# Kernel tuning notes

Measured on AMD Instinct MI355X. Metric: run time of the kernel, lower is better.

The kernel has to match this reference:

```python
import jax, jax.numpy as jnp
import numpy as np

N_NODES = 100000
N_EDGES = 1600000
IN_DIM = 128
EM_DIM = 64
HI_DIM = 64
OUT_DIM = 128
HEADS = 4


def setup_inputs() -> dict:
    key = jax.random.key(0)
    ks = jax.random.split(key, 16)
    s = 0.05  # small init scale to keep exp(a) well-conditioned
    return {
        "x_from": jax.random.normal(ks[0], (N_NODES, IN_DIM), jnp.float32),
        "edge_index": jax.random.randint(ks[1], (2, N_EDGES), 0, N_NODES, jnp.int32),
        "Wi1": jax.random.normal(ks[2], (HEADS, IN_DIM, EM_DIM), jnp.float32) * s,
        "bi1": jax.random.normal(ks[3], (HEADS, EM_DIM), jnp.float32) * s,
        "Wi2": jax.random.normal(ks[4], (HEADS, EM_DIM, EM_DIM), jnp.float32) * s,
        "bi2": jax.random.normal(ks[5], (HEADS, EM_DIM), jnp.float32) * s,
        "Wa1": jax.random.normal(ks[6], (HEADS, 2 * EM_DIM, HI_DIM), jnp.float32) * s,
        "ba1": jax.random.normal(ks[7], (HEADS, HI_DIM), jnp.float32) * s,
        "Wa2": jax.random.normal(ks[8], (HEADS, HI_DIM, 1), jnp.float32) * s,
        "ba2": jax.random.normal(ks[9], (HEADS, 1), jnp.float32) * s,
        "Wf1": jax.random.normal(ks[10], (HEADS * EM_DIM, HI_DIM), jnp.float32) * s,
        "bf1": jax.random.normal(ks[11], (HI_DIM,), jnp.float32) * s,
        "Wf2": jax.random.normal(ks[12], (HI_DIM, OUT_DIM), jnp.float32) * s,
        "bf2": jax.random.normal(ks[13], (OUT_DIM,), jnp.float32) * s,
    }


def reference(x_from, edge_index, Wi1, bi1, Wi2, bi2, Wa1, ba1, Wa2, ba2,
              Wf1, bf1, Wf2, bf2):
    n = x_from.shape[0]
    src, dst = edge_index[0], edge_index[1]

    # per-head node embedding MLP (layer_n=2, leaky_relu between layers)
    h1 = jax.nn.leaky_relu(jnp.einsum('nf,hfe->hne', x_from, Wi1) + bi1[:, None, :])
    hs = jnp.einsum('hne,hed->hnd', h1, Wi2) + bi2[:, None, :]  # [H, N, EM]
    # hs_to in the original is f_init(x_from) again -> identical to hs

    em = hs.shape[-1]
    # A(cat(h_src, h_dst)) first linear split per-node to avoid [H,E,2*EM] cat
    s_src = jnp.einsum('hne,hek->hnk', hs, Wa1[:, :em, :])  # [H, N, HI]
    s_dst = jnp.einsum('hne,hek->hnk', hs, Wa1[:, em:, :])  # [H, N, HI]
    t = jax.nn.leaky_relu(s_src[:, src] + s_dst[:, dst] + ba1[:, None, :])  # [H, E, HI]
    a = jax.nn.leaky_relu(jnp.einsum('hek,hko->heo', t, Wa2) + ba2[:, None, :])  # [H,E,1]

    e = jnp.exp(a)  # [H, E, 1]
    # softmax denominator is scatter_add over SRC (as in the source)
    e_sum = jax.vmap(lambda v: jax.ops.segment_sum(v, src, num_segments=n))(e)  # [H,N,1]
    alpha = e / e_sum[:, src]  # [H, E, 1]

    # attention-weighted aggregation: scatter_add of hs[src]*alpha onto dst
    msg = hs[:, src] * alpha  # [H, E, EM]
    agg = jax.vmap(lambda v: jax.ops.segment_sum(v, dst, num_segments=n))(msg)  # [H,N,EM]

    h_cat = jnp.transpose(agg, (1, 0, 2)).reshape(n, -1)  # [N, H*EM], head-major cat
    out = jax.nn.leaky_relu(h_cat @ Wf1 + bf1) @ Wf2 + bf2  # [N, OUT]
    return out
```

## Files before the change

kernel.cpp:

```cpp
#include <hip/hip_runtime.h>
#include <hip/hip_fp16.h>

#define NN 100000
#define NE 1600000
#define HEADS 4
#define EM 64
#define HF 256
#define IN_DIM 128
#define HI 64
#define OUT_DIM 128
#define NB_SCAN 391

using f16 = _Float16;
typedef _Float16 f16x2 __attribute__((ext_vector_type(2)));
typedef _Float16 f16x4 __attribute__((ext_vector_type(4)));
typedef float f32x4 __attribute__((ext_vector_type(4)));

__device__ __forceinline__ float lrelu(float x) { return fmaxf(x, 0.01f * x); }

__global__ __launch_bounds__(256) void k_wprep(
    const float* __restrict__ Wi1, const float* __restrict__ Wi2, const float* __restrict__ Wa1,
    uint2* __restrict__ Wi1f, uint2* __restrict__ Wi2f,
    uint2* __restrict__ Wsf, uint2* __restrict__ Wdf)
{
    int tid = blockIdx.x * 256 + threadIdx.x;
    int chunk = tid >> 6, lane = tid & 63;
    if (chunk >= 320) return;
    int g = lane >> 4, c = lane & 15;
    const float* wp;
    uint2* dst;
    if (chunk < 128) {
        int h = chunk >> 5, kc = (chunk >> 2) & 7, n = chunk & 3;
        wp = Wi1 + (size_t)h * IN_DIM * EM + (size_t)(kc * 16 + 4 * g) * EM + n * 16 + c;
        dst = Wi1f + chunk * 64 + lane;
    } else if (chunk < 192) {
        int idx = chunk - 128;
        int h = idx >> 4, kc = (idx >> 2) & 3, n = idx & 3;
        wp = Wi2 + (size_t)h * EM * EM + (size_t)(kc * 16 + 4 * g) * EM + n * 16 + c;
        dst = Wi2f + idx * 64 + lane;
    } else if (chunk < 256) {
        int idx = chunk - 192;
        int h = idx >> 4, kc = (idx >> 2) & 3, n = idx & 3;
        wp = Wa1 + (size_t)h * (2 * EM) * HI + (size_t)(kc * 16 + 4 * g) * HI + n * 16 + c;
        dst = Wsf + idx * 64 + lane;
    } else {
        int idx = chunk - 256;
        int h = idx >> 4, kc = (idx >> 2) & 3, n = idx & 3;
        wp = Wa1 + (size_t)h * (2 * EM) * HI + (size_t)(EM + kc * 16 + 4 * g) * HI + n * 16 + c;
        dst = Wdf + idx * 64 + lane;
    }
    f16x4 v = { (f16)wp[0], (f16)wp[EM], (f16)wp[2 * EM], (f16)wp[3 * EM] };
    *dst = __builtin_bit_cast(uint2, v);
}

__global__ __launch_bounds__(256) void k_embed(
    const float* __restrict__ x,
    const float* __restrict__ bi1, const float* __restrict__ bi2,
    const uint2* __restrict__ Wi1f, const uint2* __restrict__ Wi2f,
    const uint2* __restrict__ Wsf, const uint2* __restrict__ Wdf,
    const int* __restrict__ ei, int* __restrict__ cur_s, int* __restrict__ cur_d,
    f16* __restrict__ hs, f16* __restrict__ ssrc, f16* __restrict__ sdst)
{
    __shared__ __align__(16) char smem[36864];
    f16 (*xh)[136]     = (f16(*)[136])smem;
    f16 (*hsL)[32][72] = (f16(*)[32][72])smem;
    f16 (*h1L)[32][72] = (f16(*)[32][72])(smem + 18432);

    const int t = threadIdx.x;
    const int base = blockIdx.x * 32;

    {
        int tid = blockIdx.x * 256 + t;
        int e0 = tid * 2;
        #pragma unroll
        for (int j = 0; j < 2; ++j) {
            int e = e0 + j;
            if (e < NE) {
                atomicAdd(cur_s + ei[e], 1);
                atomicAdd(cur_d + ei[NE + e], 1);
            }
        }
    }

    #pragma unroll
    for (int i = 0; i < 4; ++i) {
        int q = t + i * 256;
        int row = q >> 5;
        int c4 = (q & 31) << 2;
        int gr = base + row; if (gr >= NN) gr = NN - 1;
        float4 v = *(const float4*)(x + (size_t)gr * IN_DIM + c4);
        f16x4 hv = { (f16)v.x, (f16)v.y, (f16)v.z, (f16)v.w };
        *(f16x4*)&xh[row][c4] = hv;
    }
    __syncthreads();

    const int h = t >> 6;
    const int l = t & 63;
    const int g = l >> 4;
    const int c = l & 15;

    const f32x4 z4 = { 0.f, 0.f, 0.f, 0.f };

    f32x4 acc1[2][4];
    #pragma unroll
    for (int m = 0; m < 2; ++m)
        #pragma unroll
        for (int n = 0; n < 4; ++n) acc1[m][n] = z4;
    {
        const uint2* Wf = Wi1f + (size_t)h * 32 * 64;
        for (int kc = 0; kc < 8; ++kc) {
            f16x4 bf[4];
            #pragma unroll
            for (int n = 0; n < 4; ++n)
                bf[n] = __builtin_bit_cast(f16x4, Wf[(kc * 4 + n) * 64 + l]);
            #pragma unroll
            for (int m = 0; m < 2; ++m) {
                f16x4 af = *(const f16x4*)&xh[m * 16 + c][kc * 16 + 4 * g];
                #pragma unroll
                for (int n = 0; n < 4; ++n)
                    acc1[m][n] = __builtin_amdgcn_mfma_f32_16x16x16f16(af, bf[n], acc1[m][n], 0, 0, 0);
            }
        }
    }
    __syncthreads();

    #pragma unroll
    for (int n = 0; n < 4; ++n) {
        float b = bi1[h * EM + n * 16 + c];
        #pragma unroll
        for (int m = 0; m < 2; ++m)
            #pragma unroll
            for (int r = 0; r < 4; ++r)
                h1L[h][m * 16 + 4 * g + r][n * 16 + c] = (f16)lrelu(acc1[m][n][r] + b);
    }
    __syncthreads();

    f32x4 acc2[2][4];
    #pragma unroll
    for (int m = 0; m < 2; ++m)
        #pragma unroll
        for (int n = 0; n < 4; ++n) acc2[m][n] = z4;
    {
        const uint2* Wf = Wi2f + (size_t)h * 16 * 64;
        for (int kc = 0; kc < 4; ++kc) {
            f16x4 bf[4];
            #pragma unroll
            for (int n = 0; n < 4; ++n)
                bf[n] = __builtin_bit_cast(f16x4, Wf[(kc * 4 + n) * 64 + l]);
            #pragma unroll
            for (int m = 0; m < 2; ++m) {
                f16x4 af = *(const f16x4*)&h1L[h][m * 16 + c][kc * 16 + 4 * g];
                #pragma unroll
                for (int n = 0; n < 4; ++n)
                    acc2[m][n] = __builtin_amdgcn_mfma_f32_16x16x16f16(af, bf[n], acc2[m][n], 0, 0, 0);
            }
        }
    }
    #pragma unroll
    for (int n = 0; n < 4; ++n) {
        float b = bi2[h * EM + n * 16 + c];
        #pragma unroll
        for (int m = 0; m < 2; ++m)
            #pragma unroll
            for (int r = 0; r < 4; ++r)
                hsL[h][m * 16 + 4 * g + r][n * 16 + c] = (f16)(acc2[m][n][r] + b);
    }
    __syncthreads();

    f16x4 af3[2][4];
    #pragma unroll
    for (int m = 0; m < 2; ++m)
        #pragma unroll
        for (int kc = 0; kc < 4; ++kc)
            af3[m][kc] = *(const f16x4*)&hsL[h][m * 16 + c][kc * 16 + 4 * g];

    {
        f32x4 acc3[2][4];
        #pragma unroll
        for (int m = 0; m < 2; ++m)
            #pragma unroll
            for (int n = 0; n < 4; ++n) acc3[m][n] = z4;
        const uint2* Wf = Wsf + (size_t)h * 16 * 64;
        for (int kc = 0; kc < 4; ++kc) {
            f16x4 bf[4];
            #pragma unroll
            for (int n = 0; n < 4; ++n)
                bf[n] = __builtin_bit_cast(f16x4, Wf[(kc * 4 + n) * 64 + l]);
            #pragma unroll
            for (int m = 0; m < 2; ++m)
                #pragma unroll
                for (int n = 0; n < 4; ++n)
                    acc3[m][n] = __builtin_amdgcn_mfma_f32_16x16x16f16(af3[m][kc], bf[n], acc3[m][n], 0, 0, 0);
        }
        #pragma unroll
        for (int n = 0; n < 4; ++n)
            #pragma unroll
            for (int m = 0; m < 2; ++m)
                #pragma unroll
                for (int r = 0; r < 4; ++r)
                    h1L[h][m * 16 + 4 * g + r][n * 16 + c] = (f16)acc3[m][n][r];
    }
    f32x4 acc3b[2][4];
    #pragma unroll
    for (int m = 0; m < 2; ++m)
        #pragma unroll
        for (int n = 0; n < 4; ++n) acc3b[m][n] = z4;
    {
        const uint2* Wf = Wdf + (size_t)h * 16 * 64;
        for (int kc = 0; kc < 4; ++kc) {
            f16x4 bf[4];
            #pragma unroll
            for (int n = 0; n < 4; ++n)
                bf[n] = __builtin_bit_cast(f16x4, Wf[(kc * 4 + n) * 64 + l]);
            #pragma unroll
            for (int m = 0; m < 2; ++m)
                #pragma unroll
                for (int n = 0; n < 4; ++n)
                    acc3b[m][n] = __builtin_amdgcn_mfma_f32_16x16x16f16(af3[m][kc], bf[n], acc3b[m][n], 0, 0, 0);
        }
    }
    __syncthreads();

    #pragma unroll
    for (int i = 0; i < 4; ++i) {
        int q = t + i * 256;
        int hd = q >> 8, row = (q >> 3) & 31, c8 = (q & 7) << 3;
        int node = base + row;
        if (node < NN) {
            *(int4*)&hs[(size_t)node * HF + hd * EM + c8]   = *(int4*)&hsL[hd][row][c8];
            *(int4*)&ssrc[(size_t)node * HF + hd * EM + c8] = *(int4*)&h1L[hd][row][c8];
        }
    }
    __syncthreads();

    #pragma unroll
    for (int n = 0; n < 4; ++n)
        #pragma unroll
        for (int m = 0; m < 2; ++m)
            #pragma unroll
            for (int r = 0; r < 4; ++r)
                hsL[h][m * 16 + 4 * g + r][n * 16 + c] = (f16)acc3b[m][n][r];
    __syncthreads();
    #pragma unroll
    for (int i = 0; i < 4; ++i) {
        int q = t + i * 256;
        int hd = q >> 8, row = (q >> 3) & 31, c8 = (q & 7) << 3;
        int node = base + row;
        if (node < NN)
            *(int4*)&sdst[(size_t)node * HF + hd * EM + c8] = *(int4*)&hsL[hd][row][c8];
    }
}

__global__ __launch_bounds__(256) void k_scan1(const int* __restrict__ arr0, int* __restrict__ bsum)
{
    const int t = threadIdx.x, lane = t & 63, w = t >> 6;
    const int half = (blockIdx.x >= NB_SCAN) ? 1 : 0;
    const int bb = blockIdx.x - half * NB_SCAN;
    const int* arr = arr0 + half * NN;
    int i = bb * 256 + t;
    int v = (i < NN) ? arr[i] : 0;
    #pragma unroll
    for (int d = 1; d < 64; d <<= 1) v += __shfl_xor(v, d);
    __shared__ int ws[4];
    if (lane == 0) ws[w] = v;
    __syncthreads();
    if (t == 0) bsum[blockIdx.x] = ws[0] + ws[1] + ws[2] + ws[3];
}

__global__ __launch_bounds__(256) void k_scan2(int* __restrict__ bsum0)
{
    __shared__ int wsum[4], woff[4];
    __shared__ int base, ctot;
    int* bsum = bsum0 + blockIdx.x * NB_SCAN;
    const int t = threadIdx.x, lane = t & 63, w = t >> 6;
    if (t == 0) base = 0;
    __syncthreads();
    for (int start = 0; start < NB_SCAN; start += 256) {
        int i = start + t;
        int v = (i < NB_SCAN) ? bsum[i] : 0;
        int incl = v;
        #pragma unroll
        for (int d = 1; d < 64; d <<= 1) {
            int u = __shfl_up(incl, d);
            if (lane >= d) incl += u;
        }
        if (lane == 63) wsum[w] = incl;
        __syncthreads();
        if (t == 0) {
            int s = 0;
            #pragma unroll
            for (int j = 0; j < 4; ++j) { int xv = wsum[j]; woff[j] = s; s += xv; }
            ctot = s;
        }
        __syncthreads();
        if (i < NB_SCAN) bsum[i] = base + woff[w] + incl - v;
        __syncthreads();
        if (t == 0) base += ctot;
        __syncthreads();
    }
}

__global__ __launch_bounds__(256) void k_scan3(int* __restrict__ arr0, const int* __restrict__ bsum)
{
    const int t = threadIdx.x, lane = t & 63, w = t >> 6;
    const int half = (blockIdx.x >= NB_SCAN) ? 1 : 0;
    const int bb = blockIdx.x - half * NB_SCAN;
    int* arr = arr0 + half * NN;
    int i = bb * 256 + t;
    int v = (i < NN) ? arr[i] : 0;
    int incl = v;
    #pragma unroll
    for (int d = 1; d < 64; d <<= 1) {
        int u = __shfl_up(incl, d);
        if (lane >= d) incl += u;
    }
    __shared__ int wsum[4], woff[4];
    if (lane == 63) wsum[w] = incl;
    __syncthreads();
    if (t == 0) {
        int s = 0;
        #pragma unroll
        for (int j = 0; j < 4; ++j) { int xv = wsum[j]; woff[j] = s; s += xv; }
    }
    __syncthreads();
    if (i < NN) arr[i] = bsum[blockIdx.x] + woff[w] + incl - v;
}

__global__ __launch_bounds__(256) void k_fill_src(const int* __restrict__ ei,
                                                  int* __restrict__ cur, int* __restrict__ es1)
{
    int e = blockIdx.x * 256 + threadIdx.x;
    int src = ei[e], dst = ei[NE + e];
    int pos = atomicAdd(cur + src, 1);
    es1[pos] = dst;
}

__global__ __launch_bounds__(256) void k_edge_att_csr(
    const int* __restrict__ es1, const int* __restrict__ cur_s,
    const f16* __restrict__ ssrc, const f16* __restrict__ sdst,
    const float* __restrict__ ba1, const float* __restrict__ Wa2, const float* __restrict__ ba2,
    int* __restrict__ cur_d, int* __restrict__ srcA, uint2* __restrict__ att8,
    f16* __restrict__ hs)
{
    const int wave = threadIdx.x >> 6;
    const int lane = threadIdx.x & 63;
    const int n = blockIdx.x * 4 + wave;
    const int eidx = lane >> 4;
    const int q = lane & 15;
    const int h = q >> 2;
    const int fb = q * 16;

    const int beg = (n == 0) ? 0 : cur_s[n - 1];
    const int end = cur_s[n];
    if (beg >= end) return;

    f16x2 z[8], w[8];
    {
        const int4* sr = (const int4*)(ssrc + (size_t)n * HF + fb);
        int4 s0 = sr[0], s1 = sr[1];
        const f16x2* sp0 = (const f16x2*)&s0;
        const f16x2* sp1 = (const f16x2*)&s1;
        const float4* bb = (const float4*)(ba1 + fb);
        const float4* wwp = (const float4*)(Wa2 + fb);
        #pragma unroll
        for (int j = 0; j < 4; ++j) {
            float4 b4 = bb[j];
            float4 w4 = wwp[j];
            f16x2 blo = { (f16)b4.x, (f16)b4.y }, bhi = { (f16)b4.z, (f16)b4.w };
            f16x2 wlo = { (f16)w4.x, (f16)w4.y }, whi = { (f16)w4.z, (f16)w4.w };
            f16x2 sv = (j < 2) ? sp0[2 * j] : sp1[2 * (j - 2)];
            f16x2 sv2 = (j < 2) ? sp0[2 * j + 1] : sp1[2 * (j - 2) + 1];
            z[2 * j] = sv + blo;
            z[2 * j + 1] = sv2 + bhi;
            w[2 * j] = wlo;
            w[2 * j + 1] = whi;
        }
    }
    const float ba2v = ba2[h];
    const f16x2 c001 = { (f16)0.01f, (f16)0.01f };

    float esumv = 0.f;

    int p = beg;
    int idx0 = p + eidx; if (idx0 > end - 1) idx0 = end - 1;
    bool val = (p + eidx) < end;
    int dst_cur = es1[idx0];
    const int4* dr = (const int4*)(sdst + (size_t)dst_cur * HF + fb);
    int4 d0 = dr[0], d1 = dr[1];

    while (p < end) {
        const int pn = p + 4;
        int4 nd0 = d0, nd1 = d1;
        int dst_nxt = dst_cur;
        bool val_n = false;
        if (pn < end) {
            int idx = pn + eidx; if (idx > end - 1) idx = end - 1;
            val_n = (pn + eidx) < end;
            dst_nxt = es1[idx];
            const int4* dr2 = (const int4*)(sdst + (size_t)dst_nxt * HF + fb);
            nd0 = dr2[0]; nd1 = dr2[1];
        }

        const f16x2* dp0 = (const f16x2*)&d0;
        const f16x2* dp1 = (const f16x2*)&d1;
        f16x2 pr = { (f16)0.f, (f16)0.f };
        #pragma unroll
        for (int j = 0; j < 4; ++j) {
            f16x2 u = z[j] + dp0[j];
            u = __builtin_elementwise_max(u, u * c001);
            pr += u * w[j];
        }
        #pragma unroll
        for (int j = 0; j < 4; ++j) {
            f16x2 u = z[4 + j] + dp1[j];
            u = __builtin_elementwise_max(u, u * c001);
            pr += u * w[4 + j];
        }
        float s = (float)pr.x + (float)pr.y;
        s += __shfl_xor(s, 1);
        s += __shfl_xor(s, 2);
        float a = s + ba2v;
        a = fmaxf(a, 0.01f * a);
        float eh = val ? __expf(a) : 0.f;
        esumv += eh;

        {
            int b = lane & 48;
            float e1 = __shfl(eh, b + 4);
            float e2 = __shfl(eh, b + 8);
            float e3 = __shfl(eh, b + 12);
            if (val && q == 0) {
                f16x2 p01 = { (f16)eh, (f16)e1 };
                f16x2 p23 = { (f16)e2, (f16)e3 };
                uint2 rec;
                rec.x = __builtin_bit_cast(uint, p01);
                rec.y = __builtin_bit_cast(uint, p23);
                int pos = atomicAdd(cur_d + dst_cur, 1);
                att8[pos] = rec;
                srcA[pos] = n;
            }
        }

        d0 = nd0; d1 = nd1; dst_cur = dst_nxt; val = val_n;
        p = pn;
    }

    esumv += __shfl_xor(esumv, 16);
    esumv += __shfl_xor(esumv, 32);

    if (eidx == 0) {
        float inv = 1.f / esumv;
        int4* hr = (int4*)(hs + (size_t)n * HF + fb);
        int4 h0 = hr[0], h1 = hr[1];
        f16x2* hp0 = (f16x2*)&h0;
        f16x2* hp1 = (f16x2*)&h1;
        #pragma unroll
        for (int j = 0; j < 4; ++j) {
            f16x2 v0 = hp0[j], v1 = hp1[j];
            hp0[j] = (f16x2){ (f16)((float)v0.x * inv), (f16)((float)v0.y * inv) };
            hp1[j] = (f16x2){ (f16)((float)v1.x * inv), (f16)((float)v1.y * inv) };
        }
        hr[0] = h0; hr[1] = h1;
    }
}

__global__ __launch_bounds__(256) void k_aggregate_csr(
    const int* __restrict__ srcA, const uint2* __restrict__ att8,
    const int* __restrict__ cur_d,
    const f16* __restrict__ hs,
    f16* __restrict__ agg)
{
    const int wave = threadIdx.x >> 6;
    const int lane = threadIdx.x & 63;
    const int n = blockIdx.x * 4 + wave;
    const int eidx = lane >> 4;
    const int q = lane & 15;
    const int h = q >> 2;
    const int fb = q * 16;

    const int beg = (n == 0) ? 0 : cur_d[n - 1];
    const int end = cur_d[n];

    float acc[16];
    #pragma unroll
    for (int j = 0; j < 16; ++j) acc[j] = 0.f;

#define COMP_B(a8V, hV0, hV1, valV)                                             \
    {                                                                           \
        uint sel = (h & 2) ? a8V.y : a8V.x;                                     \
        f16x2 selh = __builtin_bit_cast(f16x2, sel);                            \
        float al = valV ? (float)((h & 1) ? selh.y : selh.x) : 0.f;             \
        const f16x2* hp0 = (const f16x2*)&hV0;                                  \
        const f16x2* hp1 = (const f16x2*)&hV1;                                  \
        _Pragma("unroll")                                                       \
        for (int j = 0; j < 4; ++j) {                                           \
            f16x2 f = hp0[j];                                                   \
            acc[2 * j + 0] = fmaf((float)f.x, al, acc[2 * j + 0]);              \
            acc[2 * j + 1] = fmaf((float)f.y, al, acc[2 * j + 1]);              \
        }                                                                       \
        _Pragma("unroll")                                                       \
        for (int j = 0; j < 4; ++j) {                                           \
            f16x2 f = hp1[j];                                                   \
            acc[8 + 2 * j + 0] = fmaf((float)f.x, al, acc[8 + 2 * j + 0]);      \
            acc[8 + 2 * j + 1] = fmaf((float)f.y, al, acc[8 + 2 * j + 1]);      \
        }                                                                       \
    }

    if (beg < end) {
        int p = beg;
        int idx0 = p + eidx; if (idx0 > end - 1) idx0 = end - 1;
        bool val = (p + eidx) < end;
        int src = srcA[idx0];
        uint2 a8 = att8[idx0];
        const int4* hr = (const int4*)(hs + (size_t)src * HF + fb);
        int4 v0 = hr[0], v1 = hr[1];

        while (p < end) {
            const int pn = p + 4;
            uint2 na8 = a8;
            int4 nv0 = v0, nv1 = v1;
            bool val_n = false;
            if (pn < end) {
                int idx = pn + eidx; if (idx > end - 1) idx = end - 1;
                val_n = (pn + eidx) < end;
                int nsrc = srcA[idx];
                na8 = att8[idx];
                const int4* hr2 = (const int4*)(hs + (size_t)nsrc * HF + fb);
                nv0 = hr2[0]; nv1 = hr2[1];
            }

            COMP_B(a8, v0, v1, val);

            a8 = na8; v0 = nv0; v1 = nv1; val = val_n;
            p = pn;
        }
    }
#undef COMP_B

    #pragma unroll
    for (int j = 0; j < 16; ++j) {
        acc[j] += __shfl_xor(acc[j], 16);
        acc[j] += __shfl_xor(acc[j], 32);
    }

    if (eidx == 0) {
        int4 o0, o1;
        f16x2* op0 = (f16x2*)&o0;
        f16x2* op1 = (f16x2*)&o1;
        #pragma unroll
        for (int j = 0; j < 4; ++j) {
            op0[j] = (f16x2){ (f16)acc[2 * j], (f16)acc[2 * j + 1] };
            op1[j] = (f16x2){ (f16)acc[8 + 2 * j], (f16)acc[8 + 2 * j + 1] };
        }
        int4* ar = (int4*)(agg + (size_t)n * HF + fb);
        ar[0] = o0; ar[1] = o1;
    }
}

__global__ __launch_bounds__(256) void k_out_mlp2(
    const f16* __restrict__ agg,
    const float* __restrict__ Wf1, const float* __restrict__ bf1,
    const float* __restrict__ Wf2, const float* __restrict__ bf2,
    float* __restrict__ out)
{
    __shared__ __align__(16) f16 aggL[64][272];
    __shared__ __align__(16) f16 midL[64][72];

    const int t = threadIdx.x;
    const int base = blockIdx.x * 64;

    #pragma unroll
    for (int i = 0; i < 8; ++i) {
        int q = t + i * 256;
        int row = q >> 5, c8 = (q & 31) << 3;
        int gr = base + row; if (gr >= NN) gr = NN - 1;
        *(int4*)&aggL[row][c8] = *(const int4*)&agg[(size_t)gr * HF + c8];
    }
    __syncthreads();

    const int w = t >> 6, l = t & 63;
    const int g = l >> 4, c = l & 15;
    const f32x4 z4 = { 0.f, 0.f, 0.f, 0.f };

    {
        f32x4 acc[4] = { z4, z4, z4, z4 };
        for (int kc = 0; kc < 16; ++kc) {
            const float* wp = Wf1 + (size_t)(kc * 16 + 4 * g) * HI + w * 16 + c;
            f16x4 bf;
            bf[0] = (f16)wp[0]; bf[1] = (f16)wp[HI]; bf[2] = (f16)wp[2 * HI]; bf[3] = (f16)wp[3 * HI];
            #pragma unroll
            for (int m = 0; m < 4; ++m) {
                f16x4 af = *(const f16x4*)&aggL[m * 16 + c][kc * 16 + 4 * g];
                acc[m] = __builtin_amdgcn_mfma_f32_16x16x16f16(af, bf, acc[m], 0, 0, 0);
            }
        }
        float b = bf1[w * 16 + c];
        #pragma unroll
        for (int m = 0; m < 4; ++m)
            #pragma unroll
            for (int r = 0; r < 4; ++r)
                midL[m * 16 + 4 * g + r][w * 16 + c] = (f16)lrelu(acc[m][r] + b);
    }
    __syncthreads();

    #pragma unroll
    for (int nb = 0; nb < 2; ++nb) {
        int nt = w + nb * 4;
        f32x4 acc[4] = { z4, z4, z4, z4 };
        for (int kc = 0; kc < 4; ++kc) {
            const float* wp = Wf2 + (size_t)(kc * 16 + 4 * g) * OUT_DIM + nt * 16 + c;
            f16x4 bf;
            bf[0] = (f16)wp[0]; bf[1] = (f16)wp[OUT_DIM]; bf[2] = (f16)wp[2 * OUT_DIM]; bf[3] = (f16)wp[3 * OUT_DIM];
            #pragma unroll
            for (int m = 0; m < 4; ++m) {
                f16x4 af = *(const f16x4*)&midL[m * 16 + c][kc * 16 + 4 * g];
                acc[m] = __builtin_amdgcn_mfma_f32_16x16x16f16(af, bf, acc[m], 0, 0, 0);
            }
        }
        float b = bf2[nt * 16 + c];
        #pragma unroll
        for (int m = 0; m < 4; ++m)
            #pragma unroll
            for (int r = 0; r < 4; ++r) {
                int node = base + m * 16 + 4 * g + r;
                if (node < NN) out[(size_t)node * OUT_DIM + nt * 16 + c] = acc[m][r] + b;
            }
    }
}

extern "C" void kernel_launch(void* const* d_in, const int* in_sizes, int n_in,
                              void* d_out, int out_size, void* d_ws, size_t ws_size,
                              hipStream_t stream) {
    const float* x   = (const float*)d_in[0];
    const int*   ei  = (const int*)d_in[1];
    const float* Wi1 = (const float*)d_in[2];
    const float* bi1 = (const float*)d_in[3];
    const float* Wi2 = (const float*)d_in[4];
    const float* bi2 = (const float*)d_in[5];
    const float* Wa1 = (const float*)d_in[6];
    const float* ba1 = (const float*)d_in[7];
    const float* Wa2 = (const float*)d_in[8];
    const float* ba2 = (const float*)d_in[9];
    const float* Wf1 = (const float*)d_in[10];
    const float* bf1 = (const float*)d_in[11];
    const float* Wf2 = (const float*)d_in[12];
    const float* bf2 = (const float*)d_in[13];
    float* out = (float*)d_out;

    const size_t HS_B     = (size_t)NN * HF * sizeof(f16);
    const size_t OFF_SSRC = HS_B;
    const size_t OFF_SDST = 2 * HS_B;
    const size_t OFF_ES1  = 3 * HS_B;
    const size_t OFF_ATT  = OFF_ES1 + (size_t)NE * sizeof(int);
    const size_t OFF_SRCA = OFF_ATT + (size_t)NE * sizeof(uint2);
    const size_t OFF_CURS = OFF_SRCA + (size_t)NE * sizeof(int);
    const size_t OFF_CURD = OFF_CURS + (size_t)NN * sizeof(int);
    const size_t OFF_BSUM = OFF_CURD + (size_t)NN * sizeof(int);
    const size_t OFF_WF   = (OFF_BSUM + 2 * NB_SCAN * sizeof(int) + 15) & ~(size_t)15;
    const size_t WI1F_B = 4 * 8 * 4 * 64 * 8;
    const size_t WI2F_B = 4 * 4 * 4 * 64 * 8;
    const size_t NEED   = OFF_WF + WI1F_B + 3 * WI2F_B;
    if (ws_size < NEED) return;

    char* ws = (char*)d_ws;
    f16*   hs   = (f16*)(ws);
    f16*   ssrc = (f16*)(ws + OFF_SSRC);
    f16*   sdst = (f16*)(ws + OFF_SDST);
    int*   es1  = (int*)(ws + OFF_ES1);
    uint2* att8 = (uint2*)(ws + OFF_ATT);
    int*   srcA = (int*)(ws + OFF_SRCA);
    int*   cur_s = (int*)(ws + OFF_CURS);
    int*   cur_d = (int*)(ws + OFF_CURD);
    int*   bsum  = (int*)(ws + OFF_BSUM);
    uint2* Wi1f = (uint2*)(ws + OFF_WF);
    uint2* Wi2f = (uint2*)(ws + OFF_WF + WI1F_B);
    uint2* Wsf  = (uint2*)(ws + OFF_WF + WI1F_B + WI2F_B);
    uint2* Wdf  = (uint2*)(ws + OFF_WF + WI1F_B + 2 * WI2F_B);
    f16*   agg  = (f16*)(ws + OFF_SSRC);

    const int NB32 = NN / 32;
    const int NB64 = (NN + 63) / 64;

    (void)hipMemsetAsync(cur_s, 0, 2 * (size_t)NN * sizeof(int), stream);
    k_wprep<<<80, 256, 0, stream>>>(Wi1, Wi2, Wa1, Wi1f, Wi2f, Wsf, Wdf);
    k_embed<<<NB32, 256, 0, stream>>>(x, bi1, bi2, Wi1f, Wi2f, Wsf, Wdf,
                                      ei, cur_s, cur_d, hs, ssrc, sdst);

    k_scan1<<<2 * NB_SCAN, 256, 0, stream>>>(cur_s, bsum);
    k_scan2<<<2, 256, 0, stream>>>(bsum);
    k_scan3<<<2 * NB_SCAN, 256, 0, stream>>>(cur_s, bsum);

    k_fill_src<<<NE / 256, 256, 0, stream>>>(ei, cur_s, es1);
    k_edge_att_csr<<<NN / 4, 256, 0, stream>>>(es1, cur_s, ssrc, sdst, ba1, Wa2, ba2,
                                               cur_d, srcA, att8, hs);

    k_aggregate_csr<<<NN / 4, 256, 0, stream>>>(srcA, att8, cur_d, hs, agg);

    k_out_mlp2<<<NB64, 256, 0, stream>>>(agg, Wf1, bf1, Wf2, bf2, out);
}
```

Before: 632.7 us.

## Pack edge records, defer softmax normalization to aggregation, use fdot2

The attention kernel no longer rescales hs in place by the per-source inverse softmax sum. It stores a per-node, per-head inverse in a small inv4 array, and the aggregation kernel multiplies it in for each edge. The separate srcA and att8 edge arrays become a single 16-byte record (source id plus packed fp16 attention), placed in the output buffer as scratch. The attention dot product now uses fdot2 with fp32 accumulation, and aggregation uses packed float2 FMAs. This removes a read-modify-write pass over hs and one edge stream, at the cost of an extra scattered inv4 load per edge and slightly wider edge records.

```diff
diff --git a/kernel.cpp b/kernel.cpp
--- a/kernel.cpp
+++ b/kernel.cpp
@@ -14,6 +14,7 @@
 using f16 = _Float16;
 typedef _Float16 f16x2 __attribute__((ext_vector_type(2)));
 typedef _Float16 f16x4 __attribute__((ext_vector_type(4)));
+typedef float f32x2 __attribute__((ext_vector_type(2)));
 typedef float f32x4 __attribute__((ext_vector_type(4)));
 
 __device__ __forceinline__ float lrelu(float x) { return fmaxf(x, 0.01f * x); }
@@ -339,8 +340,7 @@
     const int* __restrict__ es1, const int* __restrict__ cur_s,
     const f16* __restrict__ ssrc, const f16* __restrict__ sdst,
     const float* __restrict__ ba1, const float* __restrict__ Wa2, const float* __restrict__ ba2,
-    int* __restrict__ cur_d, int* __restrict__ srcA, uint2* __restrict__ att8,
-    f16* __restrict__ hs)
+    int* __restrict__ cur_d, int4* __restrict__ ed16, float* __restrict__ inv4)
 {
     const int wave = threadIdx.x >> 6;
     const int lane = threadIdx.x & 63;
@@ -403,20 +403,19 @@
 
         const f16x2* dp0 = (const f16x2*)&d0;
         const f16x2* dp1 = (const f16x2*)&d1;
-        f16x2 pr = { (f16)0.f, (f16)0.f };
+        float s = 0.f;
         #pragma unroll
         for (int j = 0; j < 4; ++j) {
             f16x2 u = z[j] + dp0[j];
             u = __builtin_elementwise_max(u, u * c001);
-            pr += u * w[j];
+            s = __builtin_amdgcn_fdot2(u, w[j], s, false);
         }
         #pragma unroll
         for (int j = 0; j < 4; ++j) {
             f16x2 u = z[4 + j] + dp1[j];
             u = __builtin_elementwise_max(u, u * c001);
-            pr += u * w[4 + j];
-        }
-        float s = (float)pr.x + (float)pr.y;
+            s = __builtin_amdgcn_fdot2(u, w[4 + j], s, false);
+        }
         s += __shfl_xor(s, 1);
         s += __shfl_xor(s, 2);
         float a = s + ba2v;
@@ -432,12 +431,13 @@
             if (val && q == 0) {
                 f16x2 p01 = { (f16)eh, (f16)e1 };
                 f16x2 p23 = { (f16)e2, (f16)e3 };
-                uint2 rec;
-                rec.x = __builtin_bit_cast(uint, p01);
-                rec.y = __builtin_bit_cast(uint, p23);
+                int4 rec;
+                rec.x = n;
+                rec.y = 0;
+                rec.z = (int)__builtin_bit_cast(uint, p01);
+                rec.w = (int)__builtin_bit_cast(uint, p23);
                 int pos = atomicAdd(cur_d + dst_cur, 1);
-                att8[pos] = rec;
-                srcA[pos] = n;
+                ed16[pos] = rec;
             }
         }
 
@@ -448,25 +448,13 @@
     esumv += __shfl_xor(esumv, 16);
     esumv += __shfl_xor(esumv, 32);
 
-    if (eidx == 0) {
-        float inv = 1.f / esumv;
-        int4* hr = (int4*)(hs + (size_t)n * HF + fb);
-        int4 h0 = hr[0], h1 = hr[1];
-        f16x2* hp0 = (f16x2*)&h0;
-        f16x2* hp1 = (f16x2*)&h1;
-        #pragma unroll
-        for (int j = 0; j < 4; ++j) {
-            f16x2 v0 = hp0[j], v1 = hp1[j];
-            hp0[j] = (f16x2){ (f16)((float)v0.x * inv), (f16)((float)v0.y * inv) };
-            hp1[j] = (f16x2){ (f16)((float)v1.x * inv), (f16)((float)v1.y * inv) };
-        }
-        hr[0] = h0; hr[1] = h1;
-    }
+    if (eidx == 0 && (q & 3) == 0)
+        inv4[n * 4 + h] = 1.f / esumv;
 }
 
 __global__ __launch_bounds__(256) void k_aggregate_csr(
-    const int* __restrict__ srcA, const uint2* __restrict__ att8,
-    const int* __restrict__ cur_d,
+    const int4* __restrict__ ed16, const int* __restrict__ cur_d,
+    const float* __restrict__ inv4,
     const f16* __restrict__ hs,
     f16* __restrict__ agg)
 {
@@ -481,28 +469,31 @@
     const int beg = (n == 0) ? 0 : cur_d[n - 1];
     const int end = cur_d[n];
 
-    float acc[16];
-    #pragma unroll
-    for (int j = 0; j < 16; ++j) acc[j] = 0.f;
-
-#define COMP_B(a8V, hV0, hV1, valV)                                             \
+    const f32x2 z2 = { 0.f, 0.f };
+    f32x2 acc[8];
+    #pragma unroll
+    for (int j = 0; j < 8; ++j) acc[j] = z2;
+
+#define COMP_B(recV, ivV, hV0, hV1, valV)                                       \
     {                                                                           \
-        uint sel = (h & 2) ? a8V.y : a8V.x;                                     \
+        uint sel = (h & 2) ? (uint)recV.w : (uint)recV.z;                       \
         f16x2 selh = __builtin_bit_cast(f16x2, sel);                            \
-        float al = valV ? (float)((h & 1) ? selh.y : selh.x) : 0.f;             \
+        float att = (float)((h & 1) ? selh.y : selh.x);                         \
+        float al = valV ? att * ivV : 0.f;                                      \
+        f32x2 al2 = { al, al };                                                 \
         const f16x2* hp0 = (const f16x2*)&hV0;                                  \
         const f16x2* hp1 = (const f16x2*)&hV1;                                  \
         _Pragma("unroll")                                                       \
         for (int j = 0; j < 4; ++j) {                                           \
             f16x2 f = hp0[j];                                                   \
-            acc[2 * j + 0] = fmaf((float)f.x, al, acc[2 * j + 0]);              \
-            acc[2 * j + 1] = fmaf((float)f.y, al, acc[2 * j + 1]);              \
+            f32x2 fv = { (float)f.x, (float)f.y };                              \
+            acc[j] += fv * al2;                                                 \
         }                                                                       \
         _Pragma("unroll")                                                       \
         for (int j = 0; j < 4; ++j) {                                           \
             f16x2 f = hp1[j];                                                   \
-            acc[8 + 2 * j + 0] = fmaf((float)f.x, al, acc[8 + 2 * j + 0]);      \
-            acc[8 + 2 * j + 1] = fmaf((float)f.y, al, acc[8 + 2 * j + 1]);      \
+            f32x2 fv = { (float)f.x, (float)f.y };                              \
+            acc[4 + j] += fv * al2;                                             \
         }                                                                       \
     }
 
@@ -510,37 +501,40 @@
         int p = beg;
         int idx0 = p + eidx; if (idx0 > end - 1) idx0 = end - 1;
         bool val = (p + eidx) < end;
-        int src = srcA[idx0];
-        uint2 a8 = att8[idx0];
-        const int4* hr = (const int4*)(hs + (size_t)src * HF + fb);
+        int4 rec = ed16[idx0];
+        float iv = inv4[rec.x * 4 + h];
+        const int4* hr = (const int4*)(hs + (size_t)rec.x * HF + fb);
         int4 v0 = hr[0], v1 = hr[1];
 
         while (p < end) {
             const int pn = p + 4;
-            uint2 na8 = a8;
+            int4 nrec = rec;
+            float niv = iv;
             int4 nv0 = v0, nv1 = v1;
             bool val_n = false;
             if (pn < end) {
                 int idx = pn + eidx; if (idx > end - 1) idx = end - 1;
                 val_n = (pn + eidx) < end;
-                int nsrc = srcA[idx];
-                na8 = att8[idx];
-                const int4* hr2 = (const int4*)(hs + (size_t)nsrc * HF + fb);
+                nrec = ed16[idx];
+                niv = inv4[nrec.x * 4 + h];
+                const int4* hr2 = (const int4*)(hs + (size_t)nrec.x * HF + fb);
                 nv0 = hr2[0]; nv1 = hr2[1];
             }
 
-            COMP_B(a8, v0, v1, val);
-
-            a8 = na8; v0 = nv0; v1 = nv1; val = val_n;
+            COMP_B(rec, iv, v0, v1, val);
+
+            rec = nrec; iv = niv; v0 = nv0; v1 = nv1; val = val_n;
             p = pn;
         }
     }
 #undef COMP_B
 
     #pragma unroll
-    for (int j = 0; j < 16; ++j) {
-        acc[j] += __shfl_xor(acc[j], 16);
-        acc[j] += __shfl_xor(acc[j], 32);
+    for (int j = 0; j < 8; ++j) {
+        acc[j].x += __shfl_xor(acc[j].x, 16);
+        acc[j].x += __shfl_xor(acc[j].x, 32);
+        acc[j].y += __shfl_xor(acc[j].y, 16);
+        acc[j].y += __shfl_xor(acc[j].y, 32);
     }
 
     if (eidx == 0) {
@@ -549,8 +543,8 @@
         f16x2* op1 = (f16x2*)&o1;
         #pragma unroll
         for (int j = 0; j < 4; ++j) {
-            op0[j] = (f16x2){ (f16)acc[2 * j], (f16)acc[2 * j + 1] };
-            op1[j] = (f16x2){ (f16)acc[8 + 2 * j], (f16)acc[8 + 2 * j + 1] };
+            op0[j] = (f16x2){ (f16)acc[j].x, (f16)acc[j].y };
+            op1[j] = (f16x2){ (f16)acc[4 + j].x, (f16)acc[4 + j].y };
         }
         int4* ar = (int4*)(agg + (size_t)n * HF + fb);
         ar[0] = o0; ar[1] = o1;
@@ -651,9 +645,8 @@
     const size_t OFF_SSRC = HS_B;
     const size_t OFF_SDST = 2 * HS_B;
     const size_t OFF_ES1  = 3 * HS_B;
-    const size_t OFF_ATT  = OFF_ES1 + (size_t)NE * sizeof(int);
-    const size_t OFF_SRCA = OFF_ATT + (size_t)NE * sizeof(uint2);
-    const size_t OFF_CURS = OFF_SRCA + (size_t)NE * sizeof(int);
+    const size_t OFF_INV  = OFF_ES1 + (size_t)NE * sizeof(int);
+    const size_t OFF_CURS = OFF_INV + (size_t)NN * 4 * sizeof(float);
     const size_t OFF_CURD = OFF_CURS + (size_t)NN * sizeof(int);
     const size_t OFF_BSUM = OFF_CURD + (size_t)NN * sizeof(int);
     const size_t OFF_WF   = (OFF_BSUM + 2 * NB_SCAN * sizeof(int) + 15) & ~(size_t)15;
@@ -667,8 +660,7 @@
     f16*   ssrc = (f16*)(ws + OFF_SSRC);
     f16*   sdst = (f16*)(ws + OFF_SDST);
     int*   es1  = (int*)(ws + OFF_ES1);
-    uint2* att8 = (uint2*)(ws + OFF_ATT);
-    int*   srcA = (int*)(ws + OFF_SRCA);
+    float* inv4 = (float*)(ws + OFF_INV);
     int*   cur_s = (int*)(ws + OFF_CURS);
     int*   cur_d = (int*)(ws + OFF_CURD);
     int*   bsum  = (int*)(ws + OFF_BSUM);
@@ -677,6 +669,7 @@
     uint2* Wsf  = (uint2*)(ws + OFF_WF + WI1F_B + WI2F_B);
     uint2* Wdf  = (uint2*)(ws + OFF_WF + WI1F_B + 2 * WI2F_B);
     f16*   agg  = (f16*)(ws + OFF_SSRC);
+    int4*  ed16 = (int4*)d_out;
 
     const int NB32 = NN / 32;
     const int NB64 = (NN + 63) / 64;
@@ -692,9 +685,9 @@
 
     k_fill_src<<<NE / 256, 256, 0, stream>>>(ei, cur_s, es1);
     k_edge_att_csr<<<NN / 4, 256, 0, stream>>>(es1, cur_s, ssrc, sdst, ba1, Wa2, ba2,
-                                               cur_d, srcA, att8, hs);
-
-    k_aggregate_csr<<<NN / 4, 256, 0, stream>>>(srcA, att8, cur_d, hs, agg);
+                                               cur_d, ed16, inv4);
+
+    k_aggregate_csr<<<NN / 4, 256, 0, stream>>>(ed16, cur_d, inv4, hs, agg);
 
     k_out_mlp2<<<NB64, 256, 0, stream>>>(agg, Wf1, bf1, Wf2, bf2, out);
 }
```

New measurement: 618.0 us. -2.3%, faster.
